# Performance work log

Measured on AMD Instinct MI355X. Metric: run time of the kernel, lower is better.

## Reference

```python
import jax, jax.numpy as jnp
import numpy as np

N = 100000
E = 1600000
C_IN = 32
C_OUT = 64
B = 4
VOXEL_SIZE = 0.0625
GRID_LO, GRID_HI = 0.0, 1.0
VOX = int((GRID_HI - GRID_LO) / VOXEL_SIZE)  # 16
R_CORR = GRID_HI - GRID_LO  # r_correction = max(grid_scale) - min(grid_scale) = 1


def setup_inputs() -> dict:
    key = jax.random.key(0)
    k1, k2, k3, k4, k5, k6 = jax.random.split(key, 6)
    x = jax.random.normal(k1, (N, C_IN), dtype=jnp.float32)
    edge_index = jax.random.randint(k2, (2, E), 0, N, dtype=jnp.int32)
    pos = jax.random.uniform(k3, (N, 2), dtype=jnp.float32)
    batch = jnp.sort(jax.random.randint(k4, (N,), 0, B, dtype=jnp.int32))
    W = jax.random.normal(k5, (C_OUT, 4 * C_IN), dtype=jnp.float32) / np.sqrt(4 * C_IN)
    b = jax.random.normal(k6, (C_OUT,), dtype=jnp.float32) * 0.01
    return {"x": x, "edge_index": edge_index, "pos": pos, "batch": batch, "W": W, "b": b}


def dpo_conv(x, edge_index, pos, W, b):
    row, col = edge_index[0], edge_index[1]  # j = source, i = target (PyG default flow)
    pos_i, pos_j = pos[col], pos[row]        # [E, 2]
    v_i, v_j = x[col], x[row]                # [E, C_IN]
    diff = pos_i - pos_j                     # [E, 2]
    r2 = jnp.sum(diff * diff, axis=1, keepdims=True)  # [E, 1]
    w = diff * R_CORR / (r2 + 0.01)          # [E, 2] -> columns are diff_x, diff_y
    v_diff = v_i - v_j                       # [E, C_IN]
    # message f: [E, 3*C_IN]
    f = jnp.concatenate([v_diff * w[:, 0:1], v_diff * w[:, 1:2], v_j], axis=1)
    # scatter-mean into target nodes i = col
    summed = jax.ops.segment_sum(f, col, num_segments=N)            # [N, 3*C_IN]
    cnt = jax.ops.segment_sum(jnp.ones((E, 1), f.dtype), col, num_segments=N)
    prop = summed / jnp.maximum(cnt, 1.0)
    prop = jnp.concatenate([prop, x], axis=1)  # [N, 4*C_IN]
    return prop @ W.T + b


def reference(x, edge_index, pos, batch, W, b):
    h = jax.nn.relu(dpo_conv(x, edge_index, pos, W, b))  # [N, C_OUT]
    # voxel_grid: per-graph voxel cluster ids, then max_pool per cluster (dense grid)
    vox = jnp.clip(jnp.floor((pos - GRID_LO) / VOXEL_SIZE).astype(jnp.int32), 0, VOX - 1)
    cluster = batch * (VOX * VOX) + vox[:, 1] * VOX + vox[:, 0]     # [N]
    n_clusters = B * VOX * VOX
    pooled_x = jax.ops.segment_max(h, cluster, num_segments=n_clusters)  # [B*V^2, C_OUT]
    pooled_x = jnp.where(jnp.isfinite(pooled_x), pooled_x, 0.0)          # empty voxels -> 0
    pos_sum = jax.ops.segment_sum(pos, cluster, num_segments=n_clusters)
    node_cnt = jax.ops.segment_sum(jnp.ones((N, 1), pos.dtype), cluster, num_segments=n_clusters)
    pooled_pos = pos_sum / jnp.maximum(node_cnt, 1.0)                    # mean pos per voxel
    return pooled_x, pooled_pos, pos, batch
```

## Files before the change

kernel.cpp:

```cpp
#include <hip/hip_runtime.h>
#include <hip/hip_fp16.h>

#define NN 100000
#define NE 1600000
#define NCLUST 1024
#define OUT_POOLED_POS 65536
#define OUT_POS        67584
#define OUT_BATCH      267584

__global__ __launch_bounds__(256) void fill_kernel(const int* __restrict__ ei,
                                                   const float2* __restrict__ pos2,
                                                   int* __restrict__ wp,
                                                   uint2* __restrict__ csr64,
                                                   int cap)
{
    int t = blockIdx.x * 256 + threadIdx.x;
    int e0 = t * 4;
    if (e0 + 3 < NE) {
        int4 r = *(const int4*)(ei + e0);
        int4 c = *(const int4*)(ei + NE + e0);
        int rr[4] = {r.x, r.y, r.z, r.w};
        int cc[4] = {c.x, c.y, c.z, c.w};
        #pragma unroll
        for (int u = 0; u < 4; ++u) {
            int row = rr[u], col = cc[u];
            float2 pi = pos2[col], pj = pos2[row];
            float dx = pi.x - pj.x, dy = pi.y - pj.y;
            float inv = __builtin_amdgcn_rcpf(dx * dx + dy * dy + 0.01f);
            __half2 h2 = __floats2half2_rn(dx * inv, dy * inv);
            unsigned int wbits = *reinterpret_cast<unsigned int*>(&h2);
            int s = atomicAdd(&wp[col], 1);
            if (s < cap) csr64[(size_t)col * cap + s] = make_uint2((unsigned)row, wbits);
        }
    } else {
        for (int e = e0; e < NE; ++e) {
            int row = ei[e], col = ei[NE + e];
            float2 pi = pos2[col], pj = pos2[row];
            float dx = pi.x - pj.x, dy = pi.y - pj.y;
            float inv = __builtin_amdgcn_rcpf(dx * dx + dy * dy + 0.01f);
            __half2 h2 = __floats2half2_rn(dx * inv, dy * inv);
            unsigned int wbits = *reinterpret_cast<unsigned int*>(&h2);
            int s = atomicAdd(&wp[col], 1);
            if (s < cap) csr64[(size_t)col * cap + s] = make_uint2((unsigned)row, wbits);
        }
    }
}

__global__ __launch_bounds__(1024, 8) void fused_kernel(
    const float4* __restrict__ x4,
    const float2* __restrict__ pos2,
    const int* __restrict__ batch,
    const float4* __restrict__ W4,
    const float* __restrict__ bv,
    const int* __restrict__ wp,
    const uint2* __restrict__ csr64,
    int cap,
    float* __restrict__ out,
    float* __restrict__ pos_sum,
    float* __restrict__ node_cnt)
{
    __shared__ float4 Wt4[32 * 64];
    __shared__ float  bs[64];
    __shared__ float4 prop4[16][4][32];

    {
        int oc0 = threadIdx.x & 63;
        int k0  = threadIdx.x >> 6;
        Wt4[k0 * 64 + oc0]        = W4[oc0 * 32 + k0];
        Wt4[(k0 + 16) * 64 + oc0] = W4[oc0 * 32 + k0 + 16];
        if (threadIdx.x < 64) bs[threadIdx.x] = bv[threadIdx.x];
    }
    __syncthreads();

    const int wid  = threadIdx.x >> 6;
    const int lane = threadIdx.x & 63;
    const int q  = lane >> 4;
    const int g  = (lane >> 3) & 1;
    const int s  = lane & 7;
    const int oc = lane;
    const int nwaves = gridDim.x * 16;

    for (int wg = blockIdx.x * 16 + wid; wg * 4 < NN; wg += nwaves) {
        int n = wg * 4 + q;
        bool act = (n < NN);
        int nn = act ? n : 0;

        int cnt = wp[nn];
        int deg = act ? min(cnt, cap) : 0;
        float4 vi = x4[(size_t)nn * 8 + s];
        const uint2* bk = csr64 + (size_t)nn * cap;

        int md = deg;
        md = max(md, __shfl_xor(md, 16));
        md = max(md, __shfl_xor(md, 32));

        float a0x=0,a0y=0,a0z=0,a0w=0;
        float a1x=0,a1y=0,a1z=0,a1w=0;
        float a2x=0,a2y=0,a2z=0,a2w=0;

        int k0i = g;
        bool p0 = (k0i < deg);
        uint2 e0 = p0 ? bk[k0i] : make_uint2((unsigned)nn, 0u);
        float m0 = p0 ? 1.0f : 0.0f;
        float4 vj0 = x4[(size_t)e0.x * 8 + s];

        int k1 = g + 2;
        bool p1 = (k1 < deg);
        uint2 e1 = p1 ? bk[k1] : make_uint2((unsigned)nn, 0u);
        float m1 = p1 ? 1.0f : 0.0f;

        int iters = (md + 1) >> 1;
        for (int it = 0; it < iters; ++it) {
            int k2 = k1 + 2;
            bool p2 = (k2 < deg);
            uint2 e2 = p2 ? bk[k2] : make_uint2((unsigned)nn, 0u);
            float m2 = p2 ? 1.0f : 0.0f;
            float4 vjn = x4[(size_t)e1.x * 8 + s];

            unsigned int wb = e0.y;
            __half2 h2 = *reinterpret_cast<__half2*>(&wb);
            float2 wf = __half22float2(h2);
            float wx = wf.x, wy = wf.y;
            float vdx = vi.x - vj0.x, vdy = vi.y - vj0.y;
            float vdz = vi.z - vj0.z, vdw = vi.w - vj0.w;
            a0x += vdx * wx; a0y += vdy * wx; a0z += vdz * wx; a0w += vdw * wx;
            a1x += vdx * wy; a1y += vdy * wy; a1z += vdz * wy; a1w += vdw * wy;
            a2x += vj0.x * m0; a2y += vj0.y * m0; a2z += vj0.z * m0; a2w += vj0.w * m0;

            e0 = e1; m0 = m1; vj0 = vjn;
            e1 = e2; m1 = m2; k1 = k2;
        }

        a0x += __shfl_xor(a0x, 8); a0y += __shfl_xor(a0y, 8);
        a0z += __shfl_xor(a0z, 8); a0w += __shfl_xor(a0w, 8);
        a1x += __shfl_xor(a1x, 8); a1y += __shfl_xor(a1y, 8);
        a1z += __shfl_xor(a1z, 8); a1w += __shfl_xor(a1w, 8);
        a2x += __shfl_xor(a2x, 8); a2y += __shfl_xor(a2y, 8);
        a2z += __shfl_xor(a2z, 8); a2w += __shfl_xor(a2w, 8);

        float invd = 1.0f / fmaxf((float)cnt, 1.0f);
        if (g == 0) {
            prop4[wid][q][s]      = make_float4(a0x*invd, a0y*invd, a0z*invd, a0w*invd);
            prop4[wid][q][8 + s]  = make_float4(a1x*invd, a1y*invd, a1z*invd, a1w*invd);
            prop4[wid][q][16 + s] = make_float4(a2x*invd, a2y*invd, a2z*invd, a2w*invd);
            prop4[wid][q][24 + s] = vi;
        }
        asm volatile("s_waitcnt lgkmcnt(0)" ::: "memory");

        float bb = bs[oc];
        float acc0 = bb, acc1 = bb, acc2 = bb, acc3 = bb;
        #pragma unroll 8
        for (int k4 = 0; k4 < 32; ++k4) {
            float4 w  = Wt4[k4 * 64 + oc];
            float4 pp0 = prop4[wid][0][k4];
            float4 pp1 = prop4[wid][1][k4];
            float4 pp2 = prop4[wid][2][k4];
            float4 pp3 = prop4[wid][3][k4];
            acc0 += w.x*pp0.x + w.y*pp0.y + w.z*pp0.z + w.w*pp0.w;
            acc1 += w.x*pp1.x + w.y*pp1.y + w.z*pp1.z + w.w*pp1.w;
            acc2 += w.x*pp2.x + w.y*pp2.y + w.z*pp2.z + w.w*pp2.w;
            acc3 += w.x*pp3.x + w.y*pp3.y + w.z*pp3.z + w.w*pp3.w;
        }

        float accq[4] = {acc0, acc1, acc2, acc3};
        #pragma unroll
        for (int qq = 0; qq < 4; ++qq) {
            int n2 = wg * 4 + qq;
            if (n2 < NN) {
                float h = fmaxf(accq[qq], 0.0f);
                float2 pp = pos2[n2];
                int b = batch[n2];
                int vx = min(max((int)floorf(pp.x * 16.0f), 0), 15);
                int vy = min(max((int)floorf(pp.y * 16.0f), 0), 15);
                int cl = b * 256 + vy * 16 + vx;
                unsigned int* tgt = (unsigned int*)(out + (size_t)cl * 64 + oc);
                unsigned int prev = *tgt;
                unsigned int cur  = __float_as_uint(h);
                if (cur > prev) atomicMax(tgt, cur);
                if (oc == qq) {
                    *(float2*)(out + OUT_POS + 2 * (size_t)n2) = pp;
                    out[OUT_BATCH + n2] = (float)b;
                    atomicAdd(pos_sum + 2 * cl,     pp.x);
                    atomicAdd(pos_sum + 2 * cl + 1, pp.y);
                    atomicAdd(node_cnt + cl, 1.0f);
                }
            }
        }
        asm volatile("s_waitcnt lgkmcnt(0)" ::: "memory");
    }
}

__global__ void finalize_kernel(const float* __restrict__ pos_sum,
                                const float* __restrict__ node_cnt,
                                float* __restrict__ out_pooled_pos)
{
    int c = blockIdx.x * blockDim.x + threadIdx.x;
    if (c >= NCLUST) return;
    float inv = 1.0f / fmaxf(node_cnt[c], 1.0f);
    out_pooled_pos[2 * c]     = pos_sum[2 * c] * inv;
    out_pooled_pos[2 * c + 1] = pos_sum[2 * c + 1] * inv;
}

extern "C" void kernel_launch(void* const* d_in, const int* in_sizes, int n_in,
                              void* d_out, int out_size, void* d_ws, size_t ws_size,
                              hipStream_t stream)
{
    const float* x     = (const float*)d_in[0];
    const int*   ei    = (const int*)d_in[1];
    const float* pos   = (const float*)d_in[2];
    const int*   batch = (const int*)d_in[3];
    const float* W     = (const float*)d_in[4];
    const float* bvec  = (const float*)d_in[5];
    float* out = (float*)d_out;

    size_t fixed = (size_t)NN * sizeof(int) + 3 * NCLUST * sizeof(float);
    int cap = 48;
    if (ws_size < fixed + (size_t)NN * cap * 8) {
        cap = (int)((ws_size - fixed) / ((size_t)NN * 8));
        if (cap > 48) cap = 48;
    }

    int* wp = (int*)d_ws;
    uint2* csr64 = (uint2*)(wp + NN);
    float* pos_sum  = (float*)(csr64 + (size_t)NN * cap);
    float* node_cnt = pos_sum + 2 * NCLUST;

    hipMemsetAsync(wp, 0, NN * sizeof(int), stream);
    hipMemsetAsync(pos_sum, 0, 3 * NCLUST * sizeof(float), stream);
    hipMemsetAsync(d_out, 0, (size_t)NCLUST * 64 * sizeof(float), stream);

    fill_kernel<<<(NE / 4 + 255) / 256, 256, 0, stream>>>(
        ei, (const float2*)pos, wp, csr64, cap);

    fused_kernel<<<512, 1024, 0, stream>>>(
        (const float4*)x, (const float2*)pos, batch,
        (const float4*)W, bvec, wp, csr64, cap, out, pos_sum, node_cnt);

    finalize_kernel<<<(NCLUST + 255) / 256, 256, 0, stream>>>(
        pos_sum, node_cnt, out + NCLUST * 64);
}
```

Before: 276.5 us.

## Gather neighbor features in fp16 and batch four edge loads per iteration

Adds a pre-pass that converts x to packed fp16, so neighbor feature gathers in the aggregation loop read half the bytes. The edge loop is restructured to prefetch four CSR entries and four neighbor rows per iteration, giving more memory-level parallelism. The CSR cap is lowered from 48 to 40 to fit the extra fp16 buffer in the workspace. This trades precision on neighbor features, risks truncating high-degree nodes, and costs an extra kernel launch.

```diff
diff --git a/kernel.cpp b/kernel.cpp
--- a/kernel.cpp
+++ b/kernel.cpp
@@ -7,6 +7,26 @@
 #define OUT_POOLED_POS 65536
 #define OUT_POS        67584
 #define OUT_BATCH      267584
+
+static __device__ __forceinline__ float2 h2f(unsigned int u)
+{
+    __half2 h = *reinterpret_cast<__half2*>(&u);
+    return __half22float2(h);
+}
+
+__global__ __launch_bounds__(256) void cvt_kernel(const float4* __restrict__ x4,
+                                                  uint2* __restrict__ xh2)
+{
+    int t = blockIdx.x * 256 + threadIdx.x;
+    if (t >= NN * 8) return;
+    float4 v = x4[t];
+    __half2 lo = __floats2half2_rn(v.x, v.y);
+    __half2 hi = __floats2half2_rn(v.z, v.w);
+    uint2 o;
+    o.x = *reinterpret_cast<unsigned int*>(&lo);
+    o.y = *reinterpret_cast<unsigned int*>(&hi);
+    xh2[t] = o;
+}
 
 __global__ __launch_bounds__(256) void fill_kernel(const int* __restrict__ ei,
                                                    const float2* __restrict__ pos2,
@@ -48,6 +68,7 @@
 
 __global__ __launch_bounds__(1024, 8) void fused_kernel(
     const float4* __restrict__ x4,
+    const uint2*  __restrict__ xh2,
     const float2* __restrict__ pos2,
     const int* __restrict__ batch,
     const float4* __restrict__ W4,
@@ -98,37 +119,67 @@
         float a1x=0,a1y=0,a1z=0,a1w=0;
         float a2x=0,a2y=0,a2z=0,a2w=0;
 
-        int k0i = g;
-        bool p0 = (k0i < deg);
-        uint2 e0 = p0 ? bk[k0i] : make_uint2((unsigned)nn, 0u);
-        float m0 = p0 ? 1.0f : 0.0f;
-        float4 vj0 = x4[(size_t)e0.x * 8 + s];
-
-        int k1 = g + 2;
-        bool p1 = (k1 < deg);
-        uint2 e1 = p1 ? bk[k1] : make_uint2((unsigned)nn, 0u);
-        float m1 = p1 ? 1.0f : 0.0f;
-
-        int iters = (md + 1) >> 1;
+        int kb = g;
+        uint2 E0 = (kb     < deg) ? bk[kb]     : make_uint2((unsigned)nn, 0u);
+        uint2 E1 = (kb + 2 < deg) ? bk[kb + 2] : make_uint2((unsigned)nn, 0u);
+        uint2 E2 = (kb + 4 < deg) ? bk[kb + 4] : make_uint2((unsigned)nn, 0u);
+        uint2 E3 = (kb + 6 < deg) ? bk[kb + 6] : make_uint2((unsigned)nn, 0u);
+        uint2 X0 = xh2[(size_t)E0.x * 8 + s];
+        uint2 X1 = xh2[(size_t)E1.x * 8 + s];
+        uint2 X2 = xh2[(size_t)E2.x * 8 + s];
+        uint2 X3 = xh2[(size_t)E3.x * 8 + s];
+        unsigned int B0 = E0.y, B1 = E1.y, B2 = E2.y, B3 = E3.y;
+
+        int iters = (md + 7) >> 3;
         for (int it = 0; it < iters; ++it) {
-            int k2 = k1 + 2;
-            bool p2 = (k2 < deg);
-            uint2 e2 = p2 ? bk[k2] : make_uint2((unsigned)nn, 0u);
-            float m2 = p2 ? 1.0f : 0.0f;
-            float4 vjn = x4[(size_t)e1.x * 8 + s];
-
-            unsigned int wb = e0.y;
-            __half2 h2 = *reinterpret_cast<__half2*>(&wb);
-            float2 wf = __half22float2(h2);
-            float wx = wf.x, wy = wf.y;
-            float vdx = vi.x - vj0.x, vdy = vi.y - vj0.y;
-            float vdz = vi.z - vj0.z, vdw = vi.w - vj0.w;
-            a0x += vdx * wx; a0y += vdy * wx; a0z += vdz * wx; a0w += vdw * wx;
-            a1x += vdx * wy; a1y += vdy * wy; a1z += vdz * wy; a1w += vdw * wy;
-            a2x += vj0.x * m0; a2y += vj0.y * m0; a2z += vj0.z * m0; a2w += vj0.w * m0;
-
-            e0 = e1; m0 = m1; vj0 = vjn;
-            e1 = e2; m1 = m2; k1 = k2;
+            int nb = kb + 8;
+            uint2 F0 = (nb     < deg) ? bk[nb]     : make_uint2((unsigned)nn, 0u);
+            uint2 F1 = (nb + 2 < deg) ? bk[nb + 2] : make_uint2((unsigned)nn, 0u);
+            uint2 F2 = (nb + 4 < deg) ? bk[nb + 4] : make_uint2((unsigned)nn, 0u);
+            uint2 F3 = (nb + 6 < deg) ? bk[nb + 6] : make_uint2((unsigned)nn, 0u);
+
+            {
+                float m0 = (kb     < deg) ? 1.0f : 0.0f;
+                float m1 = (kb + 2 < deg) ? 1.0f : 0.0f;
+                float m2 = (kb + 4 < deg) ? 1.0f : 0.0f;
+                float m3 = (kb + 6 < deg) ? 1.0f : 0.0f;
+
+                float2 w0 = h2f(B0), w1 = h2f(B1), w2 = h2f(B2), w3 = h2f(B3);
+                float2 l0 = h2f(X0.x), h0 = h2f(X0.y);
+                float2 l1 = h2f(X1.x), h1 = h2f(X1.y);
+                float2 l2 = h2f(X2.x), h2_ = h2f(X2.y);
+                float2 l3 = h2f(X3.x), h3 = h2f(X3.y);
+
+                float vdx, vdy, vdz, vdw;
+                vdx = vi.x - l0.x; vdy = vi.y - l0.y; vdz = vi.z - h0.x; vdw = vi.w - h0.y;
+                a0x += vdx * w0.x; a0y += vdy * w0.x; a0z += vdz * w0.x; a0w += vdw * w0.x;
+                a1x += vdx * w0.y; a1y += vdy * w0.y; a1z += vdz * w0.y; a1w += vdw * w0.y;
+                a2x += l0.x * m0;  a2y += l0.y * m0;  a2z += h0.x * m0;  a2w += h0.y * m0;
+
+                vdx = vi.x - l1.x; vdy = vi.y - l1.y; vdz = vi.z - h1.x; vdw = vi.w - h1.y;
+                a0x += vdx * w1.x; a0y += vdy * w1.x; a0z += vdz * w1.x; a0w += vdw * w1.x;
+                a1x += vdx * w1.y; a1y += vdy * w1.y; a1z += vdz * w1.y; a1w += vdw * w1.y;
+                a2x += l1.x * m1;  a2y += l1.y * m1;  a2z += h1.x * m1;  a2w += h1.y * m1;
+
+                vdx = vi.x - l2.x; vdy = vi.y - l2.y; vdz = vi.z - h2_.x; vdw = vi.w - h2_.y;
+                a0x += vdx * w2.x; a0y += vdy * w2.x; a0z += vdz * w2.x; a0w += vdw * w2.x;
+                a1x += vdx * w2.y; a1y += vdy * w2.y; a1z += vdz * w2.y; a1w += vdw * w2.y;
+                a2x += l2.x * m2;  a2y += l2.y * m2;  a2z += h2_.x * m2; a2w += h2_.y * m2;
+
+                vdx = vi.x - l3.x; vdy = vi.y - l3.y; vdz = vi.z - h3.x; vdw = vi.w - h3.y;
+                a0x += vdx * w3.x; a0y += vdy * w3.x; a0z += vdz * w3.x; a0w += vdw * w3.x;
+                a1x += vdx * w3.y; a1y += vdy * w3.y; a1z += vdz * w3.y; a1w += vdw * w3.y;
+                a2x += l3.x * m3;  a2y += l3.y * m3;  a2z += h3.x * m3;  a2w += h3.y * m3;
+            }
+
+            if (it + 1 < iters) {
+                X0 = xh2[(size_t)F0.x * 8 + s];
+                X1 = xh2[(size_t)F1.x * 8 + s];
+                X2 = xh2[(size_t)F2.x * 8 + s];
+                X3 = xh2[(size_t)F3.x * 8 + s];
+                B0 = F0.y; B1 = F1.y; B2 = F2.y; B3 = F3.y;
+            }
+            kb = nb;
         }
 
         a0x += __shfl_xor(a0x, 8); a0y += __shfl_xor(a0y, 8);
@@ -151,7 +202,7 @@
         float acc0 = bb, acc1 = bb, acc2 = bb, acc3 = bb;
         #pragma unroll 8
         for (int k4 = 0; k4 < 32; ++k4) {
-            float4 w  = Wt4[k4 * 64 + oc];
+            float4 w   = Wt4[k4 * 64 + oc];
             float4 pp0 = prop4[wid][0][k4];
             float4 pp1 = prop4[wid][1][k4];
             float4 pp2 = prop4[wid][2][k4];
@@ -213,27 +264,30 @@
     const float* bvec  = (const float*)d_in[5];
     float* out = (float*)d_out;
 
-    size_t fixed = (size_t)NN * sizeof(int) + 3 * NCLUST * sizeof(float);
-    int cap = 48;
+    size_t fixed = (size_t)NN * 4 + (size_t)NN * 8 * 8 + 3 * NCLUST * 4;
+    int cap = 40;
     if (ws_size < fixed + (size_t)NN * cap * 8) {
         cap = (int)((ws_size - fixed) / ((size_t)NN * 8));
-        if (cap > 48) cap = 48;
+        if (cap > 40) cap = 40;
     }
 
     int* wp = (int*)d_ws;
     uint2* csr64 = (uint2*)(wp + NN);
-    float* pos_sum  = (float*)(csr64 + (size_t)NN * cap);
+    uint2* xh2 = csr64 + (size_t)NN * cap;
+    float* pos_sum  = (float*)(xh2 + (size_t)NN * 8);
     float* node_cnt = pos_sum + 2 * NCLUST;
 
     hipMemsetAsync(wp, 0, NN * sizeof(int), stream);
     hipMemsetAsync(pos_sum, 0, 3 * NCLUST * sizeof(float), stream);
     hipMemsetAsync(d_out, 0, (size_t)NCLUST * 64 * sizeof(float), stream);
 
+    cvt_kernel<<<(NN * 8 + 255) / 256, 256, 0, stream>>>((const float4*)x, xh2);
+
     fill_kernel<<<(NE / 4 + 255) / 256, 256, 0, stream>>>(
         ei, (const float2*)pos, wp, csr64, cap);
 
     fused_kernel<<<512, 1024, 0, stream>>>(
-        (const float4*)x, (const float2*)pos, batch,
+        (const float4*)x, xh2, (const float2*)pos, batch,
         (const float4*)W, bvec, wp, csr64, cap, out, pos_sum, node_cnt);
 
     finalize_kernel<<<(NCLUST + 255) / 256, 256, 0, stream>>>(
```

Result: faster. 262.0 us (-5.3%).
